# Performance work log

Hardware: AMD Instinct MI355X
Metric: run time of the kernel (lower is better)

## Reference

```python
import jax, jax.numpy as jnp
import numpy as np

HEADS = 16
KERNEL_EPS = 1e-4  # performer_pytorch softmax_kernel eps
LN_EPS = 1e-5


def layernorm(x, g, b):
    m = jnp.mean(x, axis=-1, keepdims=True)
    v = jnp.var(x, axis=-1, keepdims=True)
    return (x - m) * jax.lax.rsqrt(v + LN_EPS) * g + b


def softmax_kernel(x, proj, is_query):
    # FAVOR+ positive random features (performer_pytorch softmax_kernel)
    d = x.shape[-1]
    m = proj.shape[0]
    xn = x * (d ** -0.25)                                   # data_normalizer * data
    dd = jnp.einsum('bhnd,md->bhnm', xn, proj)              # projected logits
    diag = 0.5 * jnp.sum(xn * xn, axis=-1, keepdims=True)   # ||x||^2/2 * normalizer^2
    if is_query:
        stab = jnp.max(dd, axis=-1, keepdims=True)
    else:
        stab = jnp.max(dd, axis=(-2, -1), keepdims=True)
    return (m ** -0.5) * (jnp.exp(dd - diag - stab) + KERNEL_EPS)


def favor_attention(x, proj, Wq, bq, Wk, bk, Wv, bv, Wo, bo):
    B, N, D = x.shape
    dh = D // HEADS

    def split(t):
        return t.reshape(B, N, HEADS, dh).transpose(0, 2, 1, 3)  # b h n d

    q = split(x @ Wq.T + bq)
    k = split(x @ Wk.T + bk)
    v = split(x @ Wv.T + bv)

    qp = softmax_kernel(q, proj, True)    # b h n m
    kp = softmax_kernel(k, proj, False)   # b h n m

    # non-causal linear attention: O(n*m*d)
    ksum = kp.sum(axis=2)                                    # b h m
    d_inv = 1.0 / jnp.einsum('bhnm,bhm->bhn', qp, ksum)      # b h n
    ctx = jnp.einsum('bhnm,bhnd->bhmd', kp, v)               # b h m d
    out = jnp.einsum('bhnm,bhmd,bhn->bhnd', qp, ctx, d_inv)  # b h n d

    out = out.transpose(0, 2, 1, 3).reshape(B, N, D)
    return out @ Wo.T + bo


def reference(x, proj, ln1_g, ln1_b, Wq, bq, Wk, bk, Wv, bv, Wo, bo,
              ln2_g, ln2_b, W1, b1, W2, b2):
    depth = proj.shape[0]
    for i in range(depth):
        h = layernorm(x, ln1_g[i], ln1_b[i])
        x = x + favor_attention(h, proj[i], Wq[i], bq[i], Wk[i], bk[i],
                                Wv[i], bv[i], Wo[i], bo[i])
        h = layernorm(x, ln2_g[i], ln2_b[i])
        x = x + (jax.nn.gelu(h @ W1[i].T + b1[i], approximate=False) @ W2[i].T + b2[i])
    return x


def _orthogonal_features(rng, m, d):
    # gaussian orthogonal random matrix, scaling=1 (rows scaled by sqrt(d))
    blocks = []
    for _ in range(m // d):
        qmat, _ = np.linalg.qr(rng.standard_normal((d, d)))
        blocks.append(qmat.T)
    return (np.sqrt(d) * np.concatenate(blocks, axis=0)).astype(np.float32)


def setup_inputs() -> dict:
    B, N, D, L, M, DH = 4, 2048, 1024, 4, 256, 64
    key = jax.random.key(0)
    ks = jax.random.split(key, 8)
    rng = np.random.default_rng(0)
    proj = jnp.asarray(np.stack([_orthogonal_features(rng, M, DH) for _ in range(L)]))
    s = 0.02
    return {
        'x': jax.random.normal(ks[0], (B, N, D), jnp.float32),
        'proj': proj,
        'ln1_g': jnp.ones((L, D), jnp.float32),
        'ln1_b': jnp.zeros((L, D), jnp.float32),
        'Wq': s * jax.random.normal(ks[1], (L, D, D), jnp.float32),
        'bq': jnp.zeros((L, D), jnp.float32),
        'Wk': s * jax.random.normal(ks[2], (L, D, D), jnp.float32),
        'bk': jnp.zeros((L, D), jnp.float32),
        'Wv': s * jax.random.normal(ks[3], (L, D, D), jnp.float32),
        'bv': jnp.zeros((L, D), jnp.float32),
        'Wo': s * jax.random.normal(ks[4], (L, D, D), jnp.float32),
        'bo': jnp.zeros((L, D), jnp.float32),
        'ln2_g': jnp.ones((L, D), jnp.float32),
        'ln2_b': jnp.zeros((L, D), jnp.float32),
        'W1': s * jax.random.normal(ks[5], (L, D, D), jnp.float32),
        'b1': jnp.zeros((L, D), jnp.float32),
        'W2': s * jax.random.normal(ks[6], (L, D, D), jnp.float32),
        'b2': jnp.zeros((L, D), jnp.float32),
    }
```

## Files before the change

kernel.cpp:

```cpp
#include <hip/hip_runtime.h>

#define B_    4
#define N_    2048
#define D_    1024
#define L_    4
#define M_    256
#define DH_   64
#define H_    16
#define BH_   64
#define ROWS_ 8192
#define WN_   1048576

typedef __bf16 bf16x8 __attribute__((ext_vector_type(8)));
typedef float  f32x4  __attribute__((ext_vector_type(4)));
typedef unsigned short u16;

__device__ __forceinline__ u16 f2b(float f){
  unsigned u = __float_as_uint(f);
  u += 0x7FFFu + ((u >> 16) & 1u);
  return (u16)(u >> 16);
}
__device__ __forceinline__ float b2f(u16 h){ return __uint_as_float(((unsigned)h) << 16); }

__device__ __forceinline__ void gload16(const u16* g, u16* l){
  __builtin_amdgcn_global_load_lds(
      (const __attribute__((address_space(1))) void*)g,
      (__attribute__((address_space(3))) void*)l, 16, 0, 0);
}

__global__ __launch_bounds__(256) void wcvt_k(const float* __restrict__ s, u16* __restrict__ d, long n){
  long i = ((long)blockIdx.x*256 + threadIdx.x)*4;
  if (i+3 < n){
    float4 v = *(const float4*)(s+i);
    d[i]=f2b(v.x); d[i+1]=f2b(v.y); d[i+2]=f2b(v.z); d[i+3]=f2b(v.w);
  } else {
    for(long j=i;j<n;j++) d[j]=f2b(s[j]);
  }
}

__global__ __launch_bounds__(256) void wcvt2_k(const float* __restrict__ s, u16* __restrict__ dbase, long n){
  long i = ((long)blockIdx.x*256 + threadIdx.x)*4;
  if (i < n){
    float4 v = *(const float4*)(s+i);
    long l = i >> 20, j = i & (WN_-1);
    u16* d = dbase + l*(6l*WN_) + j;
    d[0]=f2b(v.x); d[1]=f2b(v.y); d[2]=f2b(v.z); d[3]=f2b(v.w);
  }
}

__global__ void fillf_k(float* o, long n, float v){
  long i=(long)blockIdx.x*256+threadIdx.x; if(i<n) o[i]=v;
}

__global__ __launch_bounds__(256) void ln_k(const float* __restrict__ x,
    const float* __restrict__ g, const float* __restrict__ bt, u16* __restrict__ h){
  int row = blockIdx.x, t = threadIdx.x;
  const float* xr = x + (long)row*D_;
  float4 v = *(const float4*)(xr + t*4);
  float s  = v.x+v.y+v.z+v.w;
  float ss = v.x*v.x+v.y*v.y+v.z*v.z+v.w*v.w;
  #pragma unroll
  for (int m=1;m<64;m<<=1){ s += __shfl_xor(s,m); ss += __shfl_xor(ss,m); }
  __shared__ float ps[4][2];
  int w=t>>6;
  if ((t&63)==0){ ps[w][0]=s; ps[w][1]=ss; }
  __syncthreads();
  s  = ps[0][0]+ps[1][0]+ps[2][0]+ps[3][0];
  ss = ps[0][1]+ps[1][1]+ps[2][1]+ps[3][1];
  float mean = s*(1.0f/D_);
  float rs = rsqrtf(ss*(1.0f/D_) - mean*mean + 1e-5f);
  int c=t*4;
  u16* hr = h + (long)row*D_;
  hr[c+0]=f2b((v.x-mean)*rs*g[c+0]+bt[c+0]);
  hr[c+1]=f2b((v.y-mean)*rs*g[c+1]+bt[c+1]);
  hr[c+2]=f2b((v.z-mean)*rs*g[c+2]+bt[c+2]);
  hr[c+3]=f2b((v.w-mean)*rs*g[c+3]+bt[c+3]);
}

__global__ __launch_bounds__(256) void vt_k(const u16* __restrict__ V, u16* __restrict__ Vt){
  __shared__ __align__(16) u16 ts[64][72];
  int t=threadIdx.x, z=blockIdx.y, n0=blockIdx.x*64;
  int b=z>>4, hh=z&15;
  {
    int row=t>>2, c16=(t&3)*16;
    const u16* src = V + ((long)b*N_ + n0+row)*D_ + hh*DH_ + c16;
    *(uint4*)&ts[row][c16]   = *(const uint4*)src;
    *(uint4*)&ts[row][c16+8] = *(const uint4*)(src+8);
  }
  __syncthreads();
  {
    int d=t>>2, nc=(t&3)*16;
    union { u16 u[16]; uint4 q[2]; } tmp;
    #pragma unroll
    for (int j=0;j<16;j++) tmp.u[j]=ts[nc+j][d];
    u16* dst = Vt + (long)z*DH_*N_ + (long)d*N_ + n0+nc;
    *(uint4*)dst = tmp.q[0];
    *(uint4*)(dst+8) = tmp.q[1];
  }
}

#define STAGE_PS(Ps, P) \
  _Pragma("unroll") \
  for (int i=0;i<8;i++){ \
    int c=threadIdx.x+i*256, row=c>>3, c8=c&7; \
    uint4 dv = *(const uint4*)((P) + row*64 + c8*8); \
    *(uint4*)((char*)(Ps) + (row<<7) + ((c8<<4)^((row&7)<<4))) = dv; \
  }
#define STAGE_XS_DG(Xs, X, b, hh, n0, dgL) \
  _Pragma("unroll") \
  for (int i=0;i<2;i++){ \
    int c=threadIdx.x+i*256, row=c>>3, c8=c&7; \
    uint4 dv = *(const uint4*)((X) + ((long)(b)*N_ + (n0)+row)*D_ + (hh)*DH_ + c8*8); \
    *(uint4*)((char*)(Xs) + (row<<7) + ((c8<<4)^((row&7)<<4))) = dv; \
    const u16* pe=(const u16*)&dv; \
    float sq=0.f; \
    _Pragma("unroll") \
    for (int e=0;e<8;e++){ float xv=b2f(pe[e]); sq += xv*xv; } \
    sq += __shfl_xor(sq,1); sq += __shfl_xor(sq,2); sq += __shfl_xor(sq,4); \
    if ((threadIdx.x&7)==0) (dgL)[row]=sq*0.0625f; \
  }
#define DD_MFMA(acc, Xs, Ps, w, lr, lg) \
  _Pragma("unroll") \
  for (int ks=0;ks<2;ks++){ \
    bf16x8 aF[4], bF[4]; \
    _Pragma("unroll") \
    for (int mi=0;mi<4;mi++){ \
      int row=mi*16+(lr); \
      aF[mi]=*(const bf16x8*)((const char*)(Xs) + (row<<7) + ((((ks<<2)+(lg))<<4)^((row&7)<<4))); \
    } \
    _Pragma("unroll") \
    for (int ni=0;ni<4;ni++){ \
      int row=(w)*64+ni*16+(lr); \
      bF[ni]=*(const bf16x8*)((const char*)(Ps) + (row<<7) + ((((ks<<2)+(lg))<<4)^((row&7)<<4))); \
    } \
    _Pragma("unroll") \
    for (int mi=0;mi<4;mi++) \
      _Pragma("unroll") \
      for (int ni=0;ni<4;ni++) \
        acc[mi][ni]=__builtin_amdgcn_mfma_f32_16x16x32_bf16(aF[mi],bF[ni],acc[mi][ni],0,0,0); \
  }

__global__ __launch_bounds__(256) void ddctx_k(
    const u16* __restrict__ Kb, const u16* __restrict__ P,
    const u16* __restrict__ Vt,
    float* __restrict__ part, float* __restrict__ kspart,
    float* __restrict__ msl, float* __restrict__ vsl, int zoff)
{
  __shared__ __align__(16) char smem[54784];
  u16* Ps = (u16*)smem;
  u16* Tr = (u16*)smem;
  u16* Xs = (u16*)(smem+36864);
  u16* Vs = (u16*)(smem+45056);
  float* dgL = (float*)(smem+54272);
  float* rm  = (float*)(smem+54528);
  int t=threadIdx.x, w=t>>6, lane=t&63, lr=lane&15, lg=lane>>4;
  int zl=blockIdx.y, zg=zl+zoff, slot=blockIdx.x;
  int b=zg>>4, hh=zg&15;
  const float SN = 0.35355339059327373f;

  f32x4 cacc[4][4];
  #pragma unroll
  for (int mi=0;mi<4;mi++)
    #pragma unroll
    for (int ni=0;ni<4;ni++) cacc[mi][ni]=(f32x4){0.f,0.f,0.f,0.f};
  float ksp[4]={0.f,0.f,0.f,0.f};
  float vsacc=0.f;
  float mrun=-1e30f;

  for (int s=0;s<4;++s){
    int n0 = slot*256 + s*64;
    STAGE_PS(Ps, P); STAGE_XS_DG(Xs, Kb, b, hh, n0, dgL);
    {
      int d=t>>2, nc=(t&3)*16;
      const u16* src = Vt + (long)zg*DH_*N_ + (long)d*N_ + n0 + nc;
      *(uint4*)&Vs[d*72+nc]   = *(const uint4*)src;
      *(uint4*)&Vs[d*72+nc+8] = *(const uint4*)(src+8);
    }
    __syncthreads();
    {
      int d=t>>2, q=t&3;
      float sv=0.f;
      #pragma unroll
      for (int j=0;j<16;j++) sv += b2f(Vs[d*72+q*16+j]);
      sv += __shfl_xor(sv,1); sv += __shfl_xor(sv,2);
      if (q==0) vsacc += sv;
    }
    f32x4 acc[4][4];
    #pragma unroll
    for (int mi=0;mi<4;mi++)
      #pragma unroll
      for (int ni=0;ni<4;ni++) acc[mi][ni]=(f32x4){0.f,0.f,0.f,0.f};
    DD_MFMA(acc, Xs, Ps, w, lr, lg);
    {
      float mx = acc[0][0][0];
      #pragma unroll
      for (int mi=0;mi<4;mi++)
        #pragma unroll
        for (int ni=0;ni<4;ni++)
          #pragma unroll
          for (int r=0;r<4;r++) mx=fmaxf(mx,acc[mi][ni][r]);
      #pragma unroll
      for (int m=1;m<64;m<<=1) mx = fmaxf(mx, __shfl_xor(mx,m));
      if (lane==0) rm[w]=mx;
    }
    __syncthreads();
    {
      float tm = SN*fmaxf(fmaxf(rm[0],rm[1]),fmaxf(rm[2],rm[3]));
      float nm = fmaxf(mrun, tm);
      float sc = expf(mrun - nm);
      mrun = nm;
      #pragma unroll
      for (int mi=0;mi<4;mi++)
        #pragma unroll
        for (int ni=0;ni<4;ni++)
          #pragma unroll
          for (int r=0;r<4;r++) cacc[mi][ni][r] *= sc;
      #pragma unroll
      for (int ni=0;ni<4;ni++) ksp[ni] *= sc;
    }
    #pragma unroll
    for (int mi=0;mi<4;mi++)
      #pragma unroll
      for (int ni=0;ni<4;ni++){
        int col = w*64+ni*16+lr;
        #pragma unroll
        for (int r=0;r<4;r++){
          int rw = mi*16+lg*4+r;
          float kp = 0.0625f*expf(SN*acc[mi][ni][r] - dgL[rw] - mrun);
          Tr[col*72+rw] = f2b(kp);
          ksp[ni] += kp;
        }
      }
    __syncthreads();
    #pragma unroll
    for (int ks=0;ks<2;ks++){
      bf16x8 aF[4], bF[4];
      #pragma unroll
      for (int mi=0;mi<4;mi++)
        aF[mi]=*(const bf16x8*)(Tr + (w*64+mi*16+lr)*72 + ks*32 + lg*8);
      #pragma unroll
      for (int ni=0;ni<4;ni++)
        bF[ni]=*(const bf16x8*)(Vs + (ni*16+lr)*72 + ks*32 + lg*8);
      #pragma unroll
      for (int mi=0;mi<4;mi++)
        #pragma unroll
        for (int ni=0;ni<4;ni++)
          cacc[mi][ni]=__builtin_amdgcn_mfma_f32_16x16x32_bf16(aF[mi],bF[ni],cacc[mi][ni],0,0,0);
    }
    __syncthreads();
  }
  #pragma unroll
  for (int ni=0;ni<4;ni++){
    ksp[ni] += __shfl_xor(ksp[ni],16);
    ksp[ni] += __shfl_xor(ksp[ni],32);
  }
  long sb = (long)zl*8+slot;
  if (lane<16){
    float* kb_ = kspart + sb*256;
    #pragma unroll
    for (int ni=0;ni<4;ni++) kb_[w*64+ni*16+lane] = ksp[ni];
  }
  if (t==0) msl[sb]=mrun;
  if ((t&3)==0) vsl[sb*64 + (t>>2)] = vsacc;
  float* pb = part + sb*16384;
  #pragma unroll
  for (int mi=0;mi<4;mi++)
    #pragma unroll
    for (int ni=0;ni<4;ni++){
      int d = ni*16+lr;
      #pragma unroll
      for (int r=0;r<4;r++){
        int m = w*64+mi*16+lg*4+r;
        pb[m*64+d] = cacc[mi][ni][r];
      }
    }
}

__global__ __launch_bounds__(256) void ctxred2_k(
    const float* __restrict__ part, const float* __restrict__ kspart,
    const float* __restrict__ msl, const float* __restrict__ vsl,
    u16* __restrict__ ctxT, float* __restrict__ ksm)
{
  int z = blockIdx.x, t = threadIdx.x;
  const float* pz = part + (long)z*8*16384;
  const float* kz = kspart + (long)z*8*256;
  const float* mz = msl + (long)z*8;
  const float* vz = vsl + (long)z*8*64;
  float mg = mz[0];
  #pragma unroll
  for (int s8=1;s8<8;s8++) mg = fmaxf(mg, mz[s8]);
  float scl[8];
  #pragma unroll
  for (int s8=0;s8<8;s8++) scl[s8] = expf(mz[s8]-mg);
  float s=0.f;
  #pragma unroll
  for (int s8=0;s8<8;s8++) s += kz[s8*256+t]*scl[s8];
  ksm[(long)z*256+t] = s + 0.0128f;
  __shared__ float vsT[64];
  if (t<64){
    float vv=0.f;
    #pragma unroll
    for (int s8=0;s8<8;s8++) vv += vz[s8*64+t];
    vsT[t]=vv;
  }
  __syncthreads();
  f32x4 r4[16];
  #pragma unroll
  for (int j=0;j<16;j++) r4[j]=(f32x4){0.f,0.f,0.f,0.f};
  #pragma unroll
  for (int s8=0;s8<8;s8++){
    const float* ps = pz + (long)s8*16384 + (long)t*64;
    float sc = scl[s8];
    #pragma unroll
    for (int j=0;j<16;j++){
      f32x4 v = *(const f32x4*)(ps + j*4);
      r4[j] += (f32x4){sc*v[0],sc*v[1],sc*v[2],sc*v[3]};
    }
  }
  u16 rb[64];
  #pragma unroll
  for (int j=0;j<16;j++){
    #pragma unroll
    for (int e=0;e<4;e++)
      rb[j*4+e]=f2b(r4[j][e] + 6.25e-6f*vsT[j*4+e]);
  }
  __shared__ __align__(16) u16 TT[64][72];
  u16* co = ctxT + (long)z*16384;
  for (int c=0;c<4;c++){
    __syncthreads();
    if ((t>>6)==c){
      int r=t&63;
      #pragma unroll
      for (int j=0;j<64;j+=8) *(uint4*)&TT[r][j] = *(const uint4*)&rb[j];
    }
    __syncthreads();
    int d=t>>2, mq=(t&3)*16;
    union { u16 u[16]; uint4 q[2]; } tmp;
    #pragma unroll
    for (int j=0;j<16;j++) tmp.u[j]=TT[mq+j][d];
    *(uint4*)(co + d*256 + c*64 + mq)     = tmp.q[0];
    *(uint4*)(co + d*256 + c*64 + mq + 8) = tmp.q[1];
  }
}

__global__ __launch_bounds__(256) void ddq_attn_k(
    const u16* __restrict__ Qb, const u16* __restrict__ P,
    const float* __restrict__ ksm, const u16* __restrict__ ctxT,
    u16* __restrict__ at, int zoff)
{
  __shared__ __align__(16) char smem[46336];
  u16*   Ps  = (u16*)smem;
  u16*   qpL = (u16*)smem;
  float* rdot= (float*)(smem+33792);
  float* dnvs= (float*)(smem+34816);
  u16*   Xs  = (u16*)(smem+36864);
  float* rm  = (float*)(smem+45056);
  float* dgL = (float*)(smem+46080);
  int t=threadIdx.x, w=t>>6, lane=t&63, lr=lane&15, lg=lane>>4;
  int zl=blockIdx.y, zg=zl+zoff, n0=blockIdx.x*64;
  int b=zg>>4, hh=zg&15;
  const float SN = 0.35355339059327373f;

  STAGE_PS(Ps, P); STAGE_XS_DG(Xs, Qb, b, hh, n0, dgL);
  __syncthreads();
  f32x4 acc[4][4];
  #pragma unroll
  for (int mi=0;mi<4;mi++)
    #pragma unroll
    for (int ni=0;ni<4;ni++) acc[mi][ni]=(f32x4){0.f,0.f,0.f,0.f};
  DD_MFMA(acc, Xs, Ps, w, lr, lg);
  float rmx[4][4];
  #pragma unroll
  for (int mi=0;mi<4;mi++)
    #pragma unroll
    for (int r=0;r<4;r++){
      float v = acc[mi][0][r];
      #pragma unroll
      for (int ni=1;ni<4;ni++) v=fmaxf(v, acc[mi][ni][r]);
      #pragma unroll
      for (int m=1;m<16;m<<=1) v = fmaxf(v, __shfl_xor(v,m));
      rmx[mi][r]=v;
    }
  if (lr==0){
    #pragma unroll
    for (int mi=0;mi<4;mi++)
      #pragma unroll
      for (int r=0;r<4;r++) rm[w*64 + mi*16 + lg*4 + r] = rmx[mi][r];
  }
  __syncthreads();
  const float* ksz = ksm + (long)zl*256;
  float kcol[4];
  #pragma unroll
  for (int ni=0;ni<4;ni++) kcol[ni] = ksz[w*64+ni*16+lr];
  float rd[4][4];
  #pragma unroll
  for (int mi=0;mi<4;mi++)
    #pragma unroll
    for (int r=0;r<4;r++){
      int rw = mi*16+lg*4+r;
      float st = fmaxf(fmaxf(rm[rw],rm[64+rw]),fmaxf(rm[128+rw],rm[192+rw]));
      float dgv = dgL[rw];
      float rsum = 0.f;
      #pragma unroll
      for (int ni=0;ni<4;ni++){
        int col = w*64+ni*16+lr;
        float qpv = 0.0625f*(expf(SN*acc[mi][ni][r] - dgv - SN*st) + 1e-4f);
        qpL[rw*264+col] = f2b(qpv);
        rsum += qpv*kcol[ni];
      }
      rd[mi][r]=rsum;
    }
  #pragma unroll
  for (int mi=0;mi<4;mi++)
    #pragma unroll
    for (int r=0;r<4;r++){
      #pragma unroll
      for (int m=1;m<16;m<<=1) rd[mi][r] += __shfl_xor(rd[mi][r],m);
    }
  if (lr==0){
    #pragma unroll
    for (int mi=0;mi<4;mi++)
      #pragma unroll
      for (int r=0;r<4;r++) rdot[w*64 + mi*16+lg*4+r] = rd[mi][r];
  }
  __syncthreads();
  if (t<64) dnvs[t] = 1.0f/(rdot[t]+rdot[64+t]+rdot[128+t]+rdot[192+t]);
  __syncthreads();
  const u16* cz = ctxT + (long)zl*16384;
  f32x4 aacc[4];
  #pragma unroll
  for (int ni=0;ni<4;ni++) aacc[ni]=(f32x4){0.f,0.f,0.f,0.f};
  #pragma unroll
  for (int ks=0;ks<8;ks++){
    bf16x8 aF = *(const bf16x8*)(qpL + (w*16+lr)*264 + ks*32 + lg*8);
    #pragma unroll
    for (int ni=0;ni<4;ni++){
      bf16x8 bF = *(const bf16x8*)(cz + (ni*16+lr)*256 + ks*32 + lg*8);
      aacc[ni]=__builtin_amdgcn_mfma_f32_16x16x32_bf16(aF,bF,aacc[ni],0,0,0);
    }
  }
  #pragma unroll
  for (int ni=0;ni<4;ni++){
    #pragma unroll
    for (int r=0;r<4;r++){
      int n = n0 + w*16 + lg*4 + r;
      at[((long)b*N_ + n)*D_ + hh*64 + ni*16 + lr] = f2b(aacc[ni][r]*dnvs[w*16+lg*4+r]);
    }
  }
}

template<int BM,int BN,int WR,int WC,int EPI,bool XS>
__global__ __launch_bounds__(256) void gemm_k(
    const u16* __restrict__ A, int lda,
    const u16* __restrict__ W, int ldw,
    const float* __restrict__ bias, const float* __restrict__ biasK, const float* __restrict__ biasV,
    void* __restrict__ Cv, int ldc, int K)
{
  static_assert(WR*WC==4, "4 waves");
  constexpr int WM=BM/WR, WN=BN/WC, MI=WM/16, NI=WN/16;
  __shared__ __align__(16) u16 As[BM*64];
  __shared__ __align__(16) u16 Ws[BN*64];
  int t=threadIdx.x;
  int bx, by;
  if (XS){
    unsigned gx=gridDim.x, flat=blockIdx.y*gx+blockIdx.x;
    unsigned cpx=(gx*gridDim.y)>>3;
    unsigned s=(flat&7)*cpx + (flat>>3);
    bx = s % gx; by = s / gx;
  } else { bx = blockIdx.x; by = blockIdx.y; }
  const u16* Ab = A + (long)by*BM*lda;
  const u16* Wb = W + (long)bx*BN*ldw;
  int w=t>>6, lane=t&63, lr=lane&15, lg=lane>>4;
  int wr=w/WC, wc=w%WC;
  int srow=lane>>3, swcol=((lane&7)^srow)*8;
  f32x4 acc[MI][NI];
  #pragma unroll
  for (int mi=0;mi<MI;mi++)
    #pragma unroll
    for(int ni=0;ni<NI;ni++) acc[mi][ni]=(f32x4){0.f,0.f,0.f,0.f};

  for (int k0=0;k0<K;k0+=64){
    #pragma unroll
    for (int i=0;i<BM/32;i++){
      int rb=w*(BM/4)+i*8;
      gload16(Ab + (long)(rb+srow)*lda + k0 + swcol, As + rb*64);
    }
    #pragma unroll
    for (int i=0;i<BN/32;i++){
      int rb=w*(BN/4)+i*8;
      gload16(Wb + (long)(rb+srow)*ldw + k0 + swcol, Ws + rb*64);
    }
    __syncthreads();
    #pragma unroll
    for (int ks=0;ks<2;ks++){
      bf16x8 aF[MI], bF[NI];
      #pragma unroll
      for (int mi=0;mi<MI;mi++){
        int row=wr*WM+mi*16+lr;
        aF[mi]=*(const bf16x8*)((const char*)As + (row<<7) + ((((ks<<2)+lg)<<4)^((row&7)<<4)));
      }
      #pragma unroll
      for (int ni=0;ni<NI;ni++){
        int row=wc*WN+ni*16+lr;
        bF[ni]=*(const bf16x8*)((const char*)Ws + (row<<7) + ((((ks<<2)+lg)<<4)^((row&7)<<4)));
      }
      #pragma unroll
      for (int mi=0;mi<MI;mi++)
        #pragma unroll
        for (int ni=0;ni<NI;ni++)
          acc[mi][ni]=__builtin_amdgcn_mfma_f32_16x16x32_bf16(aF[mi],bF[ni],acc[mi][ni],0,0,0);
    }
    __syncthreads();
  }

  #pragma unroll
  for (int mi=0;mi<MI;mi++){
    #pragma unroll
    for (int ni=0;ni<NI;ni++){
      int col = bx*BN + wc*WN + ni*16 + lr;
      float bv = 0.0f;
      if (EPI==6){
        int seg = col>>10;
        const float* bp = (seg==0)?bias:((seg==1)?biasK:biasV);
        bv = bp[col&1023];
      } else if (EPI<=2){
        bv = bias[col];
      }
      #pragma unroll
      for (int r=0;r<4;r++){
        int row = by*BM + wr*WM + mi*16 + lg*4 + r;
        float v = acc[mi][ni][r];
        if (EPI==0){
          ((u16*)Cv)[(long)row*ldc + col] = f2b(v+bv);
        } else if (EPI==1){
          ((float*)Cv)[(long)row*ldc + col] += v+bv;
        } else if (EPI==2){
          float u=v+bv;
          ((u16*)Cv)[(long)row*ldc + col] = f2b(0.5f*u*(1.0f+erff(u*0.70710678118654752f)));
        } else {
          int seg = col>>10, c = col&1023;
          ((u16*)Cv)[(long)seg*((long)ROWS_*D_) + (long)row*D_ + c] = f2b(v+bv);
        }
      }
    }
  }
}

struct WS {
  u16 *wbuf, *pjb, *hb, *qb, *kb, *pbuf, *sh16, *ctxT;
  float *part, *kspart, *msl, *vsl, *ksm;
  size_t total;
};
static WS plan_ws(char* base, int allW, int CH){
  WS w; size_t off=0;
  auto al=[&](size_t b)->char*{ char* p=base+off; off=(off+b+255)&~(size_t)255; return p; };
  const size_t TB=(size_t)ROWS_*D_*2;
  w.wbuf=(u16*)al((allW?6ull*L_:6ull)*WN_*2);
  w.pjb =(u16*)al((size_t)L_*M_*DH_*2);
  w.hb  =(u16*)al(TB);
  w.qb  =(u16*)al(TB);
  w.kb  =(u16*)al(TB);
  w.pbuf=(u16*)al(TB);
  w.sh16=(u16*)al(TB);
  w.part=(float*)al((size_t)CH*8*M_*DH_*4);
  w.kspart=(float*)al((size_t)CH*8*M_*4);
  w.msl =(float*)al((size_t)CH*8*4);
  w.vsl =(float*)al((size_t)CH*8*DH_*4);
  w.ctxT=(u16*)al((size_t)BH_*DH_*M_*2);
  w.ksm =(float*)al((size_t)BH_*M_*4);
  w.total=off;
  return w;
}

extern "C" void kernel_launch(void* const* d_in, const int* in_sizes, int n_in,
                              void* d_out, int out_size, void* d_ws, size_t ws_size,
                              hipStream_t stream)
{
  const float* x    = (const float*)d_in[0];
  const float* proj = (const float*)d_in[1];
  const float* ln1g = (const float*)d_in[2];
  const float* ln1b = (const float*)d_in[3];
  const float* Wq   = (const float*)d_in[4];
  const float* bq   = (const float*)d_in[5];
  const float* Wk   = (const float*)d_in[6];
  const float* bk   = (const float*)d_in[7];
  const float* Wv   = (const float*)d_in[8];
  const float* bv   = (const float*)d_in[9];
  const float* Wo   = (const float*)d_in[10];
  const float* bo   = (const float*)d_in[11];
  const float* ln2g = (const float*)d_in[12];
  const float* ln2b = (const float*)d_in[13];
  const float* W1   = (const float*)d_in[14];
  const float* b1   = (const float*)d_in[15];
  const float* W2   = (const float*)d_in[16];
  const float* b2   = (const float*)d_in[17];

  char* base=(char*)d_ws;
  int allW=1, CH=64;
  WS w = plan_ws(base, 1, 64);
  if (w.total > ws_size){ CH=16; w = plan_ws(base, 1, 16); }
  if (w.total > ws_size){ allW=0; w = plan_ws(base, 0, 16); }
  if (w.total > ws_size){
    fillf_k<<<(out_size+255)/256,256,0,stream>>>((float*)d_out,(long)out_size,(float)(ws_size>>20));
    return;
  }
  const int NCH = BH_/CH;

  u16* vb = w.pbuf;
  u16* vt = w.sh16;
  u16* at = w.hb;
  u16* tm = w.sh16;

  wcvt_k<<<(L_*M_*DH_/4+255)/256,256,0,stream>>>(proj,w.pjb,(long)L_*M_*DH_);
  if (allW){
    const long na = (long)L_*WN_;
    const int g2 = (int)(na/4/256);
    wcvt2_k<<<g2,256,0,stream>>>(Wq, w.wbuf,         na);
    wcvt2_k<<<g2,256,0,stream>>>(Wk, w.wbuf+WN_,     na);
    wcvt2_k<<<g2,256,0,stream>>>(Wv, w.wbuf+2l*WN_,  na);
    wcvt2_k<<<g2,256,0,stream>>>(Wo, w.wbuf+3l*WN_,  na);
    wcvt2_k<<<g2,256,0,stream>>>(W1, w.wbuf+4l*WN_,  na);
    wcvt2_k<<<g2,256,0,stream>>>(W2, w.wbuf+5l*WN_,  na);
  }
  hipMemcpyAsync(d_out, x, (size_t)ROWS_*D_*4, hipMemcpyDeviceToDevice, stream);
  float* Xc = (float*)d_out;

  const long wn = (long)WN_;
  const int wg = (int)(wn/4/256);
  dim3 gBig(D_/128, ROWS_/64, 1);
  dim3 gQKV(3*D_/128, ROWS_/128, 1);

  for (int l=0;l<L_;l++){
    u16* lw = w.wbuf + (allW ? (size_t)l*6*wn : 0);
    u16* wqkv=lw;  u16* wo=lw+3*wn;  u16* w1=lw+4*wn;  u16* w2=lw+5*wn;
    if (!allW){
      wcvt_k<<<wg,256,0,stream>>>(Wq+(size_t)l*wn,lw,wn);
      wcvt_k<<<wg,256,0,stream>>>(Wk+(size_t)l*wn,lw+wn,wn);
      wcvt_k<<<wg,256,0,stream>>>(Wv+(size_t)l*wn,lw+2*wn,wn);
      wcvt_k<<<wg,256,0,stream>>>(Wo+(size_t)l*wn,wo,wn);
      wcvt_k<<<wg,256,0,stream>>>(W1+(size_t)l*wn,w1,wn);
      wcvt_k<<<wg,256,0,stream>>>(W2+(size_t)l*wn,w2,wn);
    }
    const u16* pj = w.pjb + (size_t)l*M_*DH_;

    ln_k<<<ROWS_,256,0,stream>>>(Xc, ln1g+(size_t)l*D_, ln1b+(size_t)l*D_, w.hb);
    gemm_k<128,128,2,2,6,true><<<gQKV,256,0,stream>>>(w.hb,D_, wqkv,D_,
        bq+(size_t)l*D_, bk+(size_t)l*D_, bv+(size_t)l*D_, w.qb,D_,D_);
    vt_k<<<dim3(N_/64,BH_),256,0,stream>>>(vb, vt);

    for (int ch=0; ch<NCH; ch++){
      int zoff = ch*CH;
      ddctx_k<<<dim3(8,CH),256,0,stream>>>(w.kb, pj, vt, w.part, w.kspart,
                                           w.msl, w.vsl, zoff);
      ctxred2_k<<<CH,256,0,stream>>>(w.part, w.kspart, w.msl, w.vsl,
                                     w.ctxT+(long)zoff*DH_*M_, w.ksm+(long)zoff*M_);
      ddq_attn_k<<<dim3(N_/64,CH),256,0,stream>>>(w.qb, pj,
                                                  w.ksm+(long)zoff*M_,
                                                  w.ctxT+(long)zoff*DH_*M_, at, zoff);
    }

    gemm_k<64,128,1,4,1,true><<<gBig,256,0,stream>>>(at,D_, wo,D_,
        bo+(size_t)l*D_, nullptr, nullptr, Xc,D_,D_);
    ln_k<<<ROWS_,256,0,stream>>>(Xc, ln2g+(size_t)l*D_, ln2b+(size_t)l*D_, w.hb);
    gemm_k<64,128,1,4,2,true><<<gBig,256,0,stream>>>(w.hb,D_, w1,D_,
        b1+(size_t)l*D_, nullptr, nullptr, tm,D_,D_);
    gemm_k<64,128,1,4,1,true><<<gBig,256,0,stream>>>(tm,D_, w2,D_,
        b2+(size_t)l*D_, nullptr, nullptr, Xc,D_,D_);
  }
}
```

Measured before the change: 1.308 ms.

## Replace GEMM with 512-thread 256x128 tile kernel using triple-buffered async loads

```diff
diff --git a/kernel.cpp b/kernel.cpp
--- a/kernel.cpp
+++ b/kernel.cpp
@@ -449,17 +449,17 @@
   }
 }
 
-template<int BM,int BN,int WR,int WC,int EPI,bool XS>
-__global__ __launch_bounds__(256) void gemm_k(
+template<int EPI,bool XS>
+__global__ __launch_bounds__(512,2) void gemm3_k(
     const u16* __restrict__ A, int lda,
     const u16* __restrict__ W, int ldw,
     const float* __restrict__ bias, const float* __restrict__ biasK, const float* __restrict__ biasV,
     void* __restrict__ Cv, int ldc, int K)
 {
-  static_assert(WR*WC==4, "4 waves");
-  constexpr int WM=BM/WR, WN=BN/WC, MI=WM/16, NI=WN/16;
-  __shared__ __align__(16) u16 As[BM*64];
-  __shared__ __align__(16) u16 Ws[BN*64];
+  constexpr int BM=256, BN=128;
+  extern __shared__ __align__(16) u16 lds3[];
+  u16* AsB = lds3;
+  u16* BsB = lds3 + 3*BM*64;
   int t=threadIdx.x;
   int bx, by;
   if (XS){
@@ -471,68 +471,85 @@
   const u16* Ab = A + (long)by*BM*lda;
   const u16* Wb = W + (long)bx*BN*ldw;
   int w=t>>6, lane=t&63, lr=lane&15, lg=lane>>4;
-  int wr=w/WC, wc=w%WC;
+  int wr=w>>2, wc=w&3;
   int srow=lane>>3, swcol=((lane&7)^srow)*8;
-  f32x4 acc[MI][NI];
-  #pragma unroll
-  for (int mi=0;mi<MI;mi++)
-    #pragma unroll
-    for(int ni=0;ni<NI;ni++) acc[mi][ni]=(f32x4){0.f,0.f,0.f,0.f};
-
-  for (int k0=0;k0<K;k0+=64){
-    #pragma unroll
-    for (int i=0;i<BM/32;i++){
-      int rb=w*(BM/4)+i*8;
-      gload16(Ab + (long)(rb+srow)*lda + k0 + swcol, As + rb*64);
-    }
-    #pragma unroll
-    for (int i=0;i<BN/32;i++){
-      int rb=w*(BN/4)+i*8;
-      gload16(Wb + (long)(rb+srow)*ldw + k0 + swcol, Ws + rb*64);
-    }
-    __syncthreads();
-    #pragma unroll
-    for (int ks=0;ks<2;ks++){
-      bf16x8 aF[MI], bF[NI];
-      #pragma unroll
-      for (int mi=0;mi<MI;mi++){
-        int row=wr*WM+mi*16+lr;
-        aF[mi]=*(const bf16x8*)((const char*)As + (row<<7) + ((((ks<<2)+lg)<<4)^((row&7)<<4)));
-      }
-      #pragma unroll
-      for (int ni=0;ni<NI;ni++){
-        int row=wc*WN+ni*16+lr;
-        bF[ni]=*(const bf16x8*)((const char*)Ws + (row<<7) + ((((ks<<2)+lg)<<4)^((row&7)<<4)));
-      }
-      #pragma unroll
-      for (int mi=0;mi<MI;mi++)
+  f32x4 acc[8][2];
+  #pragma unroll
+  for (int mi=0;mi<8;mi++)
+    #pragma unroll
+    for (int ni=0;ni<2;ni++) acc[mi][ni]=(f32x4){0.f,0.f,0.f,0.f};
+
+  auto stage=[&](int kt, int sbuf){
+    const u16* Ak = Ab + kt*64;
+    u16* Ad = AsB + sbuf*(BM*64);
+    #pragma unroll
+    for (int i=0;i<4;i++){
+      int rb=w*32+i*8;
+      gload16(Ak + (long)(rb+srow)*lda + swcol, Ad + rb*64);
+    }
+    const u16* Bk = Wb + kt*64;
+    u16* Bd = BsB + sbuf*(BN*64);
+    #pragma unroll
+    for (int i=0;i<2;i++){
+      int rb=w*16+i*8;
+      gload16(Bk + (long)(rb+srow)*ldw + swcol, Bd + rb*64);
+    }
+  };
+
+  const int nK = K/64;
+  stage(0,0); if (nK>1) stage(1,1);
+  int rbuf=0, sbuf=2;
+  for (int kt=0; kt<nK; ++kt){
+    if (kt+1<nK) asm volatile("s_waitcnt vmcnt(6)" ::: "memory");
+    else         asm volatile("s_waitcnt vmcnt(0)" ::: "memory");
+    __builtin_amdgcn_s_barrier();
+    if (kt+2<nK) stage(kt+2, sbuf);
+    const u16* Al = AsB + rbuf*(BM*64);
+    const u16* Bl = BsB + rbuf*(BN*64);
+    bf16x8 aF[8][2], bF[2][2];
+    #pragma unroll
+    for (int ni=0;ni<2;ni++){
+      int row=wc*32+ni*16+lr;
+      #pragma unroll
+      for (int ks=0;ks<2;ks++)
+        bF[ni][ks]=*(const bf16x8*)((const char*)Bl + (row<<7) + ((((ks<<2)+lg)<<4)^((row&7)<<4)));
+    }
+    #pragma unroll
+    for (int mi=0;mi<8;mi++){
+      int row=wr*128+mi*16+lr;
+      #pragma unroll
+      for (int ks=0;ks<2;ks++)
+        aF[mi][ks]=*(const bf16x8*)((const char*)Al + (row<<7) + ((((ks<<2)+lg)<<4)^((row&7)<<4)));
+    }
+    #pragma unroll
+    for (int ks=0;ks<2;ks++)
+      #pragma unroll
+      for (int mi=0;mi<8;mi++)
         #pragma unroll
-        for (int ni=0;ni<NI;ni++)
-          acc[mi][ni]=__builtin_amdgcn_mfma_f32_16x16x32_bf16(aF[mi],bF[ni],acc[mi][ni],0,0,0);
-    }
-    __syncthreads();
-  }
-
-  #pragma unroll
-  for (int mi=0;mi<MI;mi++){
-    #pragma unroll
-    for (int ni=0;ni<NI;ni++){
-      int col = bx*BN + wc*WN + ni*16 + lr;
+        for (int ni=0;ni<2;ni++)
+          acc[mi][ni]=__builtin_amdgcn_mfma_f32_16x16x32_bf16(aF[mi][ks],bF[ni][ks],acc[mi][ni],0,0,0);
+    rbuf = (rbuf==2)?0:rbuf+1;
+    sbuf = (sbuf==2)?0:sbuf+1;
+  }
+
+  #pragma unroll
+  for (int mi=0;mi<8;mi++){
+    #pragma unroll
+    for (int ni=0;ni<2;ni++){
+      int col = bx*BN + wc*32 + ni*16 + lr;
       float bv = 0.0f;
       if (EPI==6){
         int seg = col>>10;
         const float* bp = (seg==0)?bias:((seg==1)?biasK:biasV);
         bv = bp[col&1023];
-      } else if (EPI<=2){
+      } else {
         bv = bias[col];
       }
       #pragma unroll
       for (int r=0;r<4;r++){
-        int row = by*BM + wr*WM + mi*16 + lg*4 + r;
+        int row = by*BM + wr*128 + mi*16 + lg*4 + r;
         float v = acc[mi][ni][r];
-        if (EPI==0){
-          ((u16*)Cv)[(long)row*ldc + col] = f2b(v+bv);
-        } else if (EPI==1){
+        if (EPI==1){
           ((float*)Cv)[(long)row*ldc + col] += v+bv;
         } else if (EPI==2){
           float u=v+bv;
@@ -627,8 +644,9 @@
 
   const long wn = (long)WN_;
   const int wg = (int)(wn/4/256);
-  dim3 gBig(D_/128, ROWS_/64, 1);
-  dim3 gQKV(3*D_/128, ROWS_/128, 1);
+  const size_t G3LDS = 3ull*(256+128)*64*2;
+  dim3 gBig(D_/128, ROWS_/256, 1);
+  dim3 gQKV(3*D_/128, ROWS_/256, 1);
 
   for (int l=0;l<L_;l++){
     u16* lw = w.wbuf + (allW ? (size_t)l*6*wn : 0);
@@ -644,7 +662,7 @@
     const u16* pj = w.pjb + (size_t)l*M_*DH_;
 
     ln_k<<<ROWS_,256,0,stream>>>(Xc, ln1g+(size_t)l*D_, ln1b+(size_t)l*D_, w.hb);
-    gemm_k<128,128,2,2,6,true><<<gQKV,256,0,stream>>>(w.hb,D_, wqkv,D_,
+    gemm3_k<6,true><<<gQKV,512,G3LDS,stream>>>(w.hb,D_, wqkv,D_,
         bq+(size_t)l*D_, bk+(size_t)l*D_, bv+(size_t)l*D_, w.qb,D_,D_);
     vt_k<<<dim3(N_/64,BH_),256,0,stream>>>(vb, vt);
 
@@ -659,12 +677,12 @@
                                                   w.ctxT+(long)zoff*DH_*M_, at, zoff);
     }
 
-    gemm_k<64,128,1,4,1,true><<<gBig,256,0,stream>>>(at,D_, wo,D_,
+    gemm3_k<1,true><<<gBig,512,G3LDS,stream>>>(at,D_, wo,D_,
         bo+(size_t)l*D_, nullptr, nullptr, Xc,D_,D_);
     ln_k<<<ROWS_,256,0,stream>>>(Xc, ln2g+(size_t)l*D_, ln2b+(size_t)l*D_, w.hb);
-    gemm_k<64,128,1,4,2,true><<<gBig,256,0,stream>>>(w.hb,D_, w1,D_,
+    gemm3_k<2,true><<<gBig,512,G3LDS,stream>>>(w.hb,D_, w1,D_,
         b1+(size_t)l*D_, nullptr, nullptr, tm,D_,D_);
-    gemm_k<64,128,1,4,1,true><<<gBig,256,0,stream>>>(tm,D_, w2,D_,
+    gemm3_k<1,true><<<gBig,512,G3LDS,stream>>>(tm,D_, w2,D_,
         b2+(size_t)l*D_, nullptr, nullptr, Xc,D_,D_);
   }
 }
```

After: 1.290 ms. About the same (-1.4%).
